# Performance work log

Measured on AMD Instinct MI355X. Metric: run time of the kernel, lower is better.

The kernel has to match this reference:

```python
import jax, jax.numpy as jnp
import numpy as np

BATCH = 32
N_LEVELS = (16384, 4096, 1024, 256)   # nodes at each mesh resolution
M_LEVELS = (4096, 1024, 256, 64)      # nodes after each Pool (downsample)
DEG = 6                               # directed edges per node
POOL_K = 3                            # nnz per row of downsample matrix
FILTERS = (3, 32, 32, 32, 64)         # channel chain of the 4 ChebConvs
K_CHEB = 6                            # Chebyshev polynomial order


def setup_inputs() -> dict:
    key = jax.random.key(0)
    ks = iter(jax.random.split(key, 64))
    inp = {"x": jax.random.normal(next(ks), (BATCH, N_LEVELS[0], FILTERS[0]), jnp.float32)}
    for i, N in enumerate(N_LEVELS):
        er = jnp.repeat(jnp.arange(N), DEG)
        off = jax.random.randint(next(ks), (N * DEG,), 1, N)
        inp[f"er{i}"] = er
        inp[f"ec{i}"] = (er + off) % N  # guaranteed no self loops
    for i, (M, N) in enumerate(zip(M_LEVELS, N_LEVELS)):
        inp[f"pr{i}"] = jnp.repeat(jnp.arange(M), POOL_K)
        inp[f"pc{i}"] = jax.random.randint(next(ks), (M * POOL_K,), 0, N)
        inp[f"pv{i}"] = jax.random.uniform(next(ks), (M * POOL_K,), jnp.float32)
    for i in range(4):
        fin, fout = FILTERS[i], FILTERS[i + 1]
        scale = 1.0 / np.sqrt(fin * K_CHEB)
        inp[f"W{i}"] = jax.random.normal(next(ks), (K_CHEB, fin, fout), jnp.float32) * scale
        inp[f"b{i}"] = jnp.zeros((fout,), jnp.float32)
    inp["enc_W"] = jax.random.normal(next(ks), (M_LEVELS[-1] * FILTERS[-1], 128), jnp.float32) * 0.1
    inp["enc_b"] = jnp.zeros((128,), jnp.float32)
    inp["cls_W"] = jax.random.normal(next(ks), (128, 10), jnp.float32) * 0.1
    inp["cls_b"] = jnp.zeros((10,), jnp.float32)
    return inp


def _cheb_conv(x, er, ec, W, b):
    # x: [B,N,Fin]; W: [K,Fin,Fout].
    # PyG ChebConv with lambda_max=2: L_hat = L - I = -D^{-1/2} A D^{-1/2}.
    N = x.shape[1]
    deg = jnp.zeros((N,), x.dtype).at[er].add(1.0)
    dinv = jnp.where(deg > 0, 1.0 / jnp.sqrt(jnp.maximum(deg, 1.0)), 0.0)
    norm = -(dinv[er] * dinv[ec])  # [E]

    def L(t):  # sparse matvec: gather neighbor feats, weight, scatter-add
        return jnp.zeros_like(t).at[:, er].add(t[:, ec] * norm[None, :, None])

    Tx0 = x
    out = jnp.einsum("bnf,fg->bng", Tx0, W[0])
    Tx1 = L(x)
    out = out + jnp.einsum("bnf,fg->bng", Tx1, W[1])
    for k in range(2, W.shape[0]):
        Tx2 = 2.0 * L(Tx1) - Tx0
        out = out + jnp.einsum("bnf,fg->bng", Tx2, W[k])
        Tx0, Tx1 = Tx1, Tx2
    return out + b


def _pool(x, pr, pc, pv, m):
    # sparse downsample matrix [m,N]: index_select cols * value, scatter_add rows
    B, _, F = x.shape
    return jnp.zeros((B, m, F), x.dtype).at[:, pr].add(x[:, pc] * pv[None, :, None])


def reference(x, er0, ec0, er1, ec1, er2, ec2, er3, ec3,
              pr0, pc0, pv0, pr1, pc1, pv1, pr2, pc2, pv2, pr3, pc3, pv3,
              W0, b0, W1, b1, W2, b2, W3, b3, enc_W, enc_b, cls_W, cls_b):
    ers, ecs = (er0, er1, er2, er3), (ec0, ec1, ec2, ec3)
    prs, pcs, pvs = (pr0, pr1, pr2, pr3), (pc0, pc1, pc2, pc3), (pv0, pv1, pv2, pv3)
    Ws, bs = (W0, W1, W2, W3), (b0, b1, b2, b3)
    for i in range(4):  # fixed n_layers loop (structurally distinct layers)
        x = jax.nn.relu(_cheb_conv(x, ers[i], ecs[i], Ws[i], bs[i]))
        x = _pool(x, prs[i], pcs[i], pvs[i], M_LEVELS[i])
    x = x.reshape(x.shape[0], -1)  # [B, 64*64]
    h = jax.nn.relu(x @ enc_W + enc_b)
    return h @ cls_W + cls_b
```

## Files before the change

kernel.cpp:

```cpp
#include <hip/hip_runtime.h>
#include <hip/hip_fp16.h>
#include <cstddef>
#include <cstdint>

#define BATCH 32


struct alignas(8) half4 { __half2 lo, hi; };

__device__ __forceinline__ void h4f(const half4 h, float f[4]) {
  float2 a = __half22float2(h.lo);
  float2 c = __half22float2(h.hi);
  f[0] = a.x; f[1] = a.y; f[2] = c.x; f[3] = c.y;
}
__device__ __forceinline__ void fma4(float4& a, float s, const float4& w) {
  a.x += s * w.x; a.y += s * w.y; a.z += s * w.z; a.w += s * w.w;
}
__device__ __forceinline__ float4 relu4(const float4& a) {
  return make_float4(fmaxf(a.x, 0.f), fmaxf(a.y, 0.f), fmaxf(a.z, 0.f), fmaxf(a.w, 0.f));
}

__global__ void __launch_bounds__(256) transpose_h(
    const float* __restrict__ x, half4* __restrict__ xh)
{
  int t = blockIdx.x * 256 + threadIdx.x;
  int n = t >> 5;
  int b = t & 31;
  const float* src = x + ((size_t)b * 16384 + n) * 3;
  half4 h;
  h.lo = __floats2half2_rn(src[0], src[1]);
  h.hi = __floats2half2_rn(src[2], 0.f);
  xh[t] = h;
}

__global__ void __launch_bounds__(256) cheb_step_h2(
    const half4* __restrict__ Tin, const half4* __restrict__ Tpp,
    const int* __restrict__ ec, half4* __restrict__ Tout,
    float coef, float beta)
{
  int idx = blockIdx.x * 256 + threadIdx.x;
  int n = idx >> 5;
  int b = idx & 31;
  int idx2 = idx + 262144;
  const int* e  = ec + n * 6;
  const int* e2 = ec + (n + 8192) * 6;
  float s0 = 0.f, s1 = 0.f, s2 = 0.f;
  float u0 = 0.f, u1 = 0.f, u2 = 0.f;
#pragma unroll
  for (int d = 0; d < 6; ++d) {
    half4 v = Tin[(e[d]  << 5) | b];
    half4 w = Tin[(e2[d] << 5) | b];
    float2 a = __half22float2(v.lo);
    float2 c = __half22float2(v.hi);
    s0 += a.x; s1 += a.y; s2 += c.x;
    float2 aw = __half22float2(w.lo);
    float2 cw = __half22float2(w.hi);
    u0 += aw.x; u1 += aw.y; u2 += cw.x;
  }
  half4 p  = Tpp[idx];
  half4 p2 = Tpp[idx2];
  float2 pa = __half22float2(p.lo);
  float2 pc = __half22float2(p.hi);
  float2 qa = __half22float2(p2.lo);
  float2 qc = __half22float2(p2.hi);
  half4 o, o2;
  o.lo  = __floats2half2_rn(coef * s0 + beta * pa.x, coef * s1 + beta * pa.y);
  o.hi  = __floats2half2_rn(coef * s2 + beta * pc.x, 0.f);
  o2.lo = __floats2half2_rn(coef * u0 + beta * qa.x, coef * u1 + beta * qa.y);
  o2.hi = __floats2half2_rn(coef * u2 + beta * qc.x, 0.f);
  Tout[idx]  = o;
  Tout[idx2] = o2;
}

template<int N, int M, int FOUT>
__global__ void __launch_bounds__(256) pool_conv_f3_h(
    const half4* __restrict__ Xh, const half4* __restrict__ T,
    const float* __restrict__ W, const float* __restrict__ bias,
    const int* __restrict__ pc, const float* __restrict__ pv,
    float* __restrict__ out)
{
  constexpr int F4 = FOUT / 4;
  constexpr size_t SL = (size_t)N * 32;
  __shared__ float Ws[6 * 3 * FOUT];
  for (int i = threadIdx.x; i < 6 * 3 * FOUT; i += 256) Ws[i] = W[i];
  __syncthreads();
  const float4* Ws4 = (const float4*)Ws;
  int t = blockIdx.x * 256 + threadIdx.x;
  int fo4 = t % F4;
  int b   = (t / F4) % BATCH;
  int m   = t / (F4 * BATCH);
  int c0 = pc[m * 3 + 0], c1 = pc[m * 3 + 1], c2 = pc[m * 3 + 2];
  float v0 = pv[m * 3 + 0], v1 = pv[m * 3 + 1], v2 = pv[m * 3 + 2];
  float4 bi = ((const float4*)bias)[fo4];
  float4 a0 = bi, a1 = bi, a2 = bi;
#pragma unroll
  for (int k = 0; k < 6; ++k) {
    const half4* base = (k == 0) ? Xh : (T + (size_t)(k - 1) * SL);
    float r0[4], r1[4], r2[4];
    h4f(base[(c0 << 5) | b], r0);
    h4f(base[(c1 << 5) | b], r1);
    h4f(base[(c2 << 5) | b], r2);
#pragma unroll
    for (int f = 0; f < 3; ++f) {
      float4 w = Ws4[(k * 3 + f) * F4 + fo4];
      fma4(a0, r0[f], w);
      fma4(a1, r1[f], w);
      fma4(a2, r2[f], w);
    }
  }
  a0 = relu4(a0); a1 = relu4(a1); a2 = relu4(a2);
  float4 acc;
  acc.x = v0*a0.x + v1*a1.x + v2*a2.x;
  acc.y = v0*a0.y + v1*a1.y + v2*a2.y;
  acc.z = v0*a0.z + v1*a1.z + v2*a2.z;
  acc.w = v0*a0.w + v1*a1.w + v2*a2.w;
  ((float4*)out)[((size_t)m * BATCH + b) * F4 + fo4] = acc;
}

template<int N, int F, int THREADS, int MINW>
__global__ void __launch_bounds__(THREADS, MINW) cheb_recur_hh(
    const float* __restrict__ X,
    const int* __restrict__ ec,
    __half* __restrict__ Th)
{
  constexpr int NPT = N / THREADS;
  __shared__ half4 cur[N];
  const float cI = -1.0f / 6.0f;
  const float cS = -1.0f / 3.0f;
  const int b = blockIdx.x & 31;
  const int fbase = (blockIdx.x >> 5) * 4;
  constexpr size_t SLH = (size_t)N * 32 * F;
  half4 prevv[NPT], newh[NPT];
#pragma unroll
  for (int i = 0; i < NPT; ++i) {
    int n = threadIdx.x + i * THREADS;
    float4 xv = *(const float4*)(X + ((size_t)n * 32 + b) * F + fbase);
    half4 h;
    h.lo = __floats2half2_rn(xv.x, xv.y);
    h.hi = __floats2half2_rn(xv.z, xv.w);
    cur[n] = h;
  }
  __syncthreads();
#pragma unroll 1
  for (int k = 1; k <= 5; ++k) {
    __half* Tk = Th + (size_t)(k - 1) * SLH;
#pragma unroll
    for (int i = 0; i < NPT; ++i) {
      int n = threadIdx.x + i * THREADS;
      const int2* e2 = (const int2*)(ec + n * 6);
      int2 ea = e2[0], eb = e2[1], ez = e2[2];
      int na[6];
      na[0] = ea.x; na[1] = ea.y; na[2] = eb.x;
      na[3] = eb.y; na[4] = ez.x; na[5] = ez.y;
      float s0 = 0.f, s1 = 0.f, s2 = 0.f, s3 = 0.f;
#pragma unroll
      for (int d = 0; d < 6; ++d) {
        half4 t = cur[na[d]];
        float2 a = __half22float2(t.lo);
        float2 c = __half22float2(t.hi);
        s0 += a.x; s1 += a.y; s2 += c.x; s3 += c.y;
      }
      float v0, v1, v2, v3;
      if (k == 1) {
        v0 = cI * s0; v1 = cI * s1; v2 = cI * s2; v3 = cI * s3;
      } else {
        float2 pa = __half22float2(prevv[i].lo);
        float2 pc = __half22float2(prevv[i].hi);
        v0 = cS * s0 - pa.x; v1 = cS * s1 - pa.y;
        v2 = cS * s2 - pc.x; v3 = cS * s3 - pc.y;
      }
      half4 h;
      h.lo = __floats2half2_rn(v0, v1);
      h.hi = __floats2half2_rn(v2, v3);
      newh[i] = h;
      *(half4*)(Tk + ((size_t)n * 32 + b) * F + fbase) = h;
    }
    __syncthreads();
#pragma unroll
    for (int i = 0; i < NPT; ++i) {
      int n = threadIdx.x + i * THREADS;
      prevv[i] = cur[n];
      cur[n] = newh[i];
    }
    __syncthreads();
  }
}

template<int N, int M, int FOUT, bool OUT_BM>
__global__ void __launch_bounds__(256) pool_conv_v32_h(
    const float* __restrict__ X, const __half* __restrict__ Th,
    const float* __restrict__ W, const float* __restrict__ bias,
    const int* __restrict__ pc, const float* __restrict__ pv,
    float* __restrict__ out)
{
  constexpr int FIN = 32;
  constexpr int F4 = FOUT / 4;
  constexpr size_t SLH = (size_t)N * 32 * FIN;
  __shared__ float Ws[6 * FIN * FOUT];
  for (int i = threadIdx.x; i < 6 * FIN * FOUT; i += 256) Ws[i] = W[i];
  __syncthreads();
  const float4* Ws4 = (const float4*)Ws;
  const float4* X4p = (const float4*)X;
  int t = blockIdx.x * 256 + threadIdx.x;
  int fo4 = t % F4;
  int b   = (t / F4) % BATCH;
  int m   = t / (F4 * BATCH);
  int c0 = pc[m * 3 + 0], c1 = pc[m * 3 + 1], c2 = pc[m * 3 + 2];
  float v0 = pv[m * 3 + 0], v1 = pv[m * 3 + 1], v2 = pv[m * 3 + 2];
  float4 bi = ((const float4*)bias)[fo4];
  float4 a0 = bi, a1 = bi, a2 = bi;
  {
    const float4* r0 = X4p + ((size_t)c0 * BATCH + b) * 8;
    const float4* r1 = X4p + ((size_t)c1 * BATCH + b) * 8;
    const float4* r2 = X4p + ((size_t)c2 * BATCH + b) * 8;
#pragma unroll
    for (int fi = 0; fi < 8; ++fi) {
      float4 t0 = r0[fi], t1 = r1[fi], t2 = r2[fi];
#pragma unroll
      for (int ff = 0; ff < 4; ++ff) {
        float4 w = Ws4[(fi * 4 + ff) * F4 + fo4];
        fma4(a0, ((const float*)&t0)[ff], w);
        fma4(a1, ((const float*)&t1)[ff], w);
        fma4(a2, ((const float*)&t2)[ff], w);
      }
    }
  }
#pragma unroll 1
  for (int k = 1; k < 6; ++k) {
    const half4* base = (const half4*)(Th + (size_t)(k - 1) * SLH);
    const half4* r0 = base + ((size_t)c0 * 32 + b) * 8;
    const half4* r1 = base + ((size_t)c1 * 32 + b) * 8;
    const half4* r2 = base + ((size_t)c2 * 32 + b) * 8;
#pragma unroll
    for (int q = 0; q < 8; ++q) {
      float f0[4], f1[4], f2[4];
      h4f(r0[q], f0); h4f(r1[q], f1); h4f(r2[q], f2);
#pragma unroll
      for (int ff = 0; ff < 4; ++ff) {
        float4 w = Ws4[((k * 32) + q * 4 + ff) * F4 + fo4];
        fma4(a0, f0[ff], w);
        fma4(a1, f1[ff], w);
        fma4(a2, f2[ff], w);
      }
    }
  }
  a0 = relu4(a0); a1 = relu4(a1); a2 = relu4(a2);
  float4 acc;
  acc.x = v0*a0.x + v1*a1.x + v2*a2.x;
  acc.y = v0*a0.y + v1*a1.y + v2*a2.y;
  acc.z = v0*a0.z + v1*a1.z + v2*a2.z;
  acc.w = v0*a0.w + v1*a1.w + v2*a2.w;
  size_t oi = OUT_BM ? (((size_t)b * M + m) * F4 + fo4) : (((size_t)m * BATCH + b) * F4 + fo4);
  ((float4*)out)[oi] = acc;
}

__global__ void __launch_bounds__(128) encoder_partial_ws(
    const float* __restrict__ Xf, const float* __restrict__ encW,
    float* __restrict__ partial)
{
  int j  = blockIdx.x;
  int fo = threadIdx.x;
  int i0 = j * 32;
  float w[32];
#pragma unroll
  for (int i = 0; i < 32; ++i) w[i] = encW[(size_t)(i0 + i) * 128 + fo];
#pragma unroll 1
  for (int b = 0; b < 32; ++b) {
    const float* xr = Xf + b * 4096 + i0;
    float s = 0.f;
#pragma unroll
    for (int i = 0; i < 32; ++i) s += xr[i] * w[i];
    partial[((size_t)b * 128 + j) * 128 + fo] = s;
  }
}

__global__ void __launch_bounds__(128) encoder_reduce_cls(
    const float* __restrict__ partial, const float* __restrict__ encB,
    const float* __restrict__ clsW, const float* __restrict__ clsB,
    float* __restrict__ out)
{
  int b = blockIdx.x;
  int fo = threadIdx.x;
  float acc = encB[fo];
#pragma unroll 8
  for (int j = 0; j < 128; ++j) acc += partial[((size_t)b * 128 + j) * 128 + fo];
  __shared__ float Hs[128];
  Hs[fo] = fmaxf(acc, 0.f);
  __syncthreads();
  if (fo < 10) {
    float s = clsB[fo];
#pragma unroll 4
    for (int f = 0; f < 128; ++f) s += Hs[f] * clsW[f * 10 + fo];
    out[b * 10 + fo] = s;
  }
}

extern "C" void kernel_launch(void* const* d_in, const int* in_sizes, int n_in,
                              void* d_out, int out_size, void* d_ws, size_t ws_size,
                              hipStream_t stream)
{
  const float* x   = (const float*)d_in[0];
  const int* ec0 = (const int*)d_in[2];
  const int* ec1 = (const int*)d_in[4];
  const int* ec2 = (const int*)d_in[6];
  const int* ec3 = (const int*)d_in[8];
  const int* pc0 = (const int*)d_in[10]; const float* pv0 = (const float*)d_in[11];
  const int* pc1 = (const int*)d_in[13]; const float* pv1 = (const float*)d_in[14];
  const int* pc2 = (const int*)d_in[16]; const float* pv2 = (const float*)d_in[17];
  const int* pc3 = (const int*)d_in[19]; const float* pv3 = (const float*)d_in[20];
  const float* W0 = (const float*)d_in[21]; const float* b0 = (const float*)d_in[22];
  const float* W1 = (const float*)d_in[23]; const float* b1 = (const float*)d_in[24];
  const float* W2 = (const float*)d_in[25]; const float* b2 = (const float*)d_in[26];
  const float* W3 = (const float*)d_in[27]; const float* b3 = (const float*)d_in[28];
  const float* encW = (const float*)d_in[29]; const float* encB = (const float*)d_in[30];
  const float* clsW = (const float*)d_in[31]; const float* clsB = (const float*)d_in[32];
  float* out = (float*)d_out;

  float* ws = (float*)d_ws;
  half4*  Xh = (half4*)ws;
  __half* Th = (__half*)(ws + 1048576);
  float* X1 = ws + 1048576 + 10485760;
  float* X2 = X1 + 4194304;
  float* X3 = X2 + 1048576;
  float* X4 = X3 + 262144;
  float* P  = X4 + 131072;

  const float cI = -1.0f / 6.0f;
  const float cS = -1.0f / 3.0f;
  dim3 blk(256);

  transpose_h<<<dim3(2048), blk, 0, stream>>>(x, Xh);

  {
    constexpr size_t S = (size_t)16384 * 32;
    half4* T4 = (half4*)Th;
    cheb_step_h2<<<dim3(1024), blk, 0, stream>>>(Xh,       Xh,       ec0, T4,        cI,  0.f);
    cheb_step_h2<<<dim3(1024), blk, 0, stream>>>(T4,       Xh,       ec0, T4 + S,    cS, -1.f);
    cheb_step_h2<<<dim3(1024), blk, 0, stream>>>(T4 + S,   T4,       ec0, T4 + 2*S,  cS, -1.f);
    cheb_step_h2<<<dim3(1024), blk, 0, stream>>>(T4 + 2*S, T4 + S,   ec0, T4 + 3*S,  cS, -1.f);
    cheb_step_h2<<<dim3(1024), blk, 0, stream>>>(T4 + 3*S, T4 + 2*S, ec0, T4 + 4*S,  cS, -1.f);
    pool_conv_f3_h<16384, 4096, 32><<<dim3(4096), blk, 0, stream>>>(
        Xh, (const half4*)Th, W0, b0, pc0, pv0, X1);
  }
  cheb_recur_hh<4096, 32, 1024, 4><<<dim3(256), dim3(1024), 0, stream>>>(X1, ec1, Th);
  pool_conv_v32_h<4096, 1024, 32, false><<<dim3(1024), blk, 0, stream>>>(
      X1, Th, W1, b1, pc1, pv1, X2);

  cheb_recur_hh<1024, 32, 256, 4><<<dim3(256), blk, 0, stream>>>(X2, ec2, Th);
  pool_conv_v32_h<1024, 256, 32, false><<<dim3(256), blk, 0, stream>>>(
      X2, Th, W2, b2, pc2, pv2, X3);

  cheb_recur_hh<256, 32, 256, 4><<<dim3(256), blk, 0, stream>>>(X3, ec3, Th);
  pool_conv_v32_h<256, 64, 64, true><<<dim3(128), blk, 0, stream>>>(
      X3, Th, W3, b3, pc3, pv3, X4);

  encoder_partial_ws<<<dim3(128), dim3(128), 0, stream>>>(X4, encW, P);
  encoder_reduce_cls<<<dim3(32), dim3(128), 0, stream>>>(P, encB, clsW, clsB, out);
}
```

Before: 281.7 us.

## Fuse all post-level-1 stages into one per-batch persistent tail kernel

Replaces the level-1 pool, the level-2/3 Chebyshev recurrences and pools, and both encoder kernels with a single 32-block kernel, one block per batch element. Each block handles all feature slabs sequentially and uses block-level barriers instead of kernel boundaries. The level-0 cheb step goes back to one node per thread with vectorised int2 edge loads, and the level-3 weights are stored in shared memory as fp16. This removes about eight kernel launches and their idle gaps, but runs the tail on only 32 CUs, which serialises work that was previously spread over 256 blocks.

```diff
diff --git a/kernel.cpp b/kernel.cpp
--- a/kernel.cpp
+++ b/kernel.cpp
@@ -33,7 +33,7 @@
   xh[t] = h;
 }
 
-__global__ void __launch_bounds__(256) cheb_step_h2(
+__global__ void __launch_bounds__(256) cheb_step_h(
     const half4* __restrict__ Tin, const half4* __restrict__ Tpp,
     const int* __restrict__ ec, half4* __restrict__ Tout,
     float coef, float beta)
@@ -41,48 +41,38 @@
   int idx = blockIdx.x * 256 + threadIdx.x;
   int n = idx >> 5;
   int b = idx & 31;
-  int idx2 = idx + 262144;
-  const int* e  = ec + n * 6;
-  const int* e2 = ec + (n + 8192) * 6;
+  const int2* e2 = (const int2*)(ec + n * 6);
+  int2 ea = e2[0], eb = e2[1], ez = e2[2];
+  int na[6];
+  na[0] = ea.x; na[1] = ea.y; na[2] = eb.x;
+  na[3] = eb.y; na[4] = ez.x; na[5] = ez.y;
   float s0 = 0.f, s1 = 0.f, s2 = 0.f;
-  float u0 = 0.f, u1 = 0.f, u2 = 0.f;
 #pragma unroll
   for (int d = 0; d < 6; ++d) {
-    half4 v = Tin[(e[d]  << 5) | b];
-    half4 w = Tin[(e2[d] << 5) | b];
+    half4 v = Tin[(na[d] << 5) | b];
     float2 a = __half22float2(v.lo);
     float2 c = __half22float2(v.hi);
     s0 += a.x; s1 += a.y; s2 += c.x;
-    float2 aw = __half22float2(w.lo);
-    float2 cw = __half22float2(w.hi);
-    u0 += aw.x; u1 += aw.y; u2 += cw.x;
-  }
-  half4 p  = Tpp[idx];
-  half4 p2 = Tpp[idx2];
+  }
+  half4 p = Tpp[idx];
   float2 pa = __half22float2(p.lo);
   float2 pc = __half22float2(p.hi);
-  float2 qa = __half22float2(p2.lo);
-  float2 qc = __half22float2(p2.hi);
-  half4 o, o2;
-  o.lo  = __floats2half2_rn(coef * s0 + beta * pa.x, coef * s1 + beta * pa.y);
-  o.hi  = __floats2half2_rn(coef * s2 + beta * pc.x, 0.f);
-  o2.lo = __floats2half2_rn(coef * u0 + beta * qa.x, coef * u1 + beta * qa.y);
-  o2.hi = __floats2half2_rn(coef * u2 + beta * qc.x, 0.f);
-  Tout[idx]  = o;
-  Tout[idx2] = o2;
-}
-
-template<int N, int M, int FOUT>
+  half4 o;
+  o.lo = __floats2half2_rn(coef * s0 + beta * pa.x, coef * s1 + beta * pa.y);
+  o.hi = __floats2half2_rn(coef * s2 + beta * pc.x, 0.f);
+  Tout[idx] = o;
+}
+
 __global__ void __launch_bounds__(256) pool_conv_f3_h(
     const half4* __restrict__ Xh, const half4* __restrict__ T,
     const float* __restrict__ W, const float* __restrict__ bias,
     const int* __restrict__ pc, const float* __restrict__ pv,
     float* __restrict__ out)
 {
-  constexpr int F4 = FOUT / 4;
-  constexpr size_t SL = (size_t)N * 32;
-  __shared__ float Ws[6 * 3 * FOUT];
-  for (int i = threadIdx.x; i < 6 * 3 * FOUT; i += 256) Ws[i] = W[i];
+  constexpr int F4 = 8;
+  constexpr size_t SL = (size_t)16384 * 32;
+  __shared__ float Ws[576];
+  for (int i = threadIdx.x; i < 576; i += 256) Ws[i] = W[i];
   __syncthreads();
   const float4* Ws4 = (const float4*)Ws;
   int t = blockIdx.x * 256 + threadIdx.x;
@@ -117,10 +107,75 @@
   ((float4*)out)[((size_t)m * BATCH + b) * F4 + fo4] = acc;
 }
 
+template<int N, int M, int FOUT, bool OUT_BM, bool WH>
+__device__ __forceinline__ void st_pool32(
+    const float* __restrict__ X, const __half* __restrict__ Th,
+    const void* __restrict__ Ws, const float* __restrict__ bias,
+    const int* __restrict__ pc, const float* __restrict__ pv,
+    float* __restrict__ out, int t)
+{
+  constexpr int F4 = FOUT / 4;
+  constexpr size_t SLH = (size_t)N * 32 * 32;
+  const float4* Wsf = (const float4*)Ws;
+  const half4* Wsh = (const half4*)Ws;
+  const float4* X4p = (const float4*)X;
+  int fo4 = t % F4;
+  int b   = (t / F4) % BATCH;
+  int m   = t / (F4 * BATCH);
+  int c0 = pc[m * 3 + 0], c1 = pc[m * 3 + 1], c2 = pc[m * 3 + 2];
+  float v0 = pv[m * 3 + 0], v1 = pv[m * 3 + 1], v2 = pv[m * 3 + 2];
+  float4 bi = ((const float4*)bias)[fo4];
+  float4 a0 = bi, a1 = bi, a2 = bi;
+#define WGET(off) (WH ? ({ float wf[4]; h4f(Wsh[off], wf); make_float4(wf[0],wf[1],wf[2],wf[3]); }) : Wsf[off])
+  {
+    const float4* r0 = X4p + ((size_t)c0 * BATCH + b) * 8;
+    const float4* r1 = X4p + ((size_t)c1 * BATCH + b) * 8;
+    const float4* r2 = X4p + ((size_t)c2 * BATCH + b) * 8;
+#pragma unroll
+    for (int fi = 0; fi < 8; ++fi) {
+      float4 t0 = r0[fi], t1 = r1[fi], t2 = r2[fi];
+#pragma unroll
+      for (int ff = 0; ff < 4; ++ff) {
+        float4 w = WGET((fi * 4 + ff) * F4 + fo4);
+        fma4(a0, ((const float*)&t0)[ff], w);
+        fma4(a1, ((const float*)&t1)[ff], w);
+        fma4(a2, ((const float*)&t2)[ff], w);
+      }
+    }
+  }
+#pragma unroll 1
+  for (int k = 1; k < 6; ++k) {
+    const half4* base = (const half4*)(Th + (size_t)(k - 1) * SLH);
+    const half4* r0 = base + ((size_t)c0 * 32 + b) * 8;
+    const half4* r1 = base + ((size_t)c1 * 32 + b) * 8;
+    const half4* r2 = base + ((size_t)c2 * 32 + b) * 8;
+#pragma unroll
+    for (int q = 0; q < 8; ++q) {
+      float f0[4], f1[4], f2[4];
+      h4f(r0[q], f0); h4f(r1[q], f1); h4f(r2[q], f2);
+#pragma unroll
+      for (int ff = 0; ff < 4; ++ff) {
+        float4 w = WGET(((k * 32) + q * 4 + ff) * F4 + fo4);
+        fma4(a0, f0[ff], w);
+        fma4(a1, f1[ff], w);
+        fma4(a2, f2[ff], w);
+      }
+    }
+  }
+#undef WGET
+  a0 = relu4(a0); a1 = relu4(a1); a2 = relu4(a2);
+  float4 acc;
+  acc.x = v0*a0.x + v1*a1.x + v2*a2.x;
+  acc.y = v0*a0.y + v1*a1.y + v2*a2.y;
+  acc.z = v0*a0.z + v1*a1.z + v2*a2.z;
+  acc.w = v0*a0.w + v1*a1.w + v2*a2.w;
+  size_t oi = OUT_BM ? (((size_t)b * M + m) * F4 + fo4) : (((size_t)m * BATCH + b) * F4 + fo4);
+  ((float4*)out)[oi] = acc;
+}
+
 template<int N, int F, int THREADS, int MINW>
 __global__ void __launch_bounds__(THREADS, MINW) cheb_recur_hh(
-    const float* __restrict__ X,
-    const int* __restrict__ ec,
+    const float* __restrict__ X, const int* __restrict__ ec,
     __half* __restrict__ Th)
 {
   constexpr int NPT = N / THREADS;
@@ -186,114 +241,155 @@
   }
 }
 
-template<int N, int M, int FOUT, bool OUT_BM>
-__global__ void __launch_bounds__(256) pool_conv_v32_h(
-    const float* __restrict__ X, const __half* __restrict__ Th,
-    const float* __restrict__ W, const float* __restrict__ bias,
-    const int* __restrict__ pc, const float* __restrict__ pv,
-    float* __restrict__ out)
-{
-  constexpr int FIN = 32;
-  constexpr int F4 = FOUT / 4;
-  constexpr size_t SLH = (size_t)N * 32 * FIN;
-  __shared__ float Ws[6 * FIN * FOUT];
-  for (int i = threadIdx.x; i < 6 * FIN * FOUT; i += 256) Ws[i] = W[i];
-  __syncthreads();
-  const float4* Ws4 = (const float4*)Ws;
-  const float4* X4p = (const float4*)X;
-  int t = blockIdx.x * 256 + threadIdx.x;
-  int fo4 = t % F4;
-  int b   = (t / F4) % BATCH;
-  int m   = t / (F4 * BATCH);
-  int c0 = pc[m * 3 + 0], c1 = pc[m * 3 + 1], c2 = pc[m * 3 + 2];
-  float v0 = pv[m * 3 + 0], v1 = pv[m * 3 + 1], v2 = pv[m * 3 + 2];
-  float4 bi = ((const float4*)bias)[fo4];
-  float4 a0 = bi, a1 = bi, a2 = bi;
+template<int N>
+__device__ void tail_recur(const float* __restrict__ X, const int* __restrict__ ec,
+                           __half* __restrict__ Th, half4* cur, int b, int fbase, int tid)
+{
+  constexpr size_t SLH = (size_t)N * 32 * 32;
+  const float cI = -1.0f / 6.0f;
+  const float cS = -1.0f / 3.0f;
+  const bool act = tid < N;
+  const int n = tid;
+  half4 prev, neww;
+  if (act) {
+    float4 xv = *(const float4*)(X + ((size_t)n * 32 + b) * 32 + fbase);
+    half4 h;
+    h.lo = __floats2half2_rn(xv.x, xv.y);
+    h.hi = __floats2half2_rn(xv.z, xv.w);
+    cur[n] = h;
+  }
+  __syncthreads();
+#pragma unroll 1
+  for (int k = 1; k <= 5; ++k) {
+    __half* Tk = Th + (size_t)(k - 1) * SLH;
+    if (act) {
+      const int2* e2 = (const int2*)(ec + n * 6);
+      int2 ea = e2[0], eb = e2[1], ez = e2[2];
+      int na[6];
+      na[0] = ea.x; na[1] = ea.y; na[2] = eb.x;
+      na[3] = eb.y; na[4] = ez.x; na[5] = ez.y;
+      float s0 = 0.f, s1 = 0.f, s2 = 0.f, s3 = 0.f;
+#pragma unroll
+      for (int d = 0; d < 6; ++d) {
+        half4 t = cur[na[d]];
+        float2 a = __half22float2(t.lo);
+        float2 c = __half22float2(t.hi);
+        s0 += a.x; s1 += a.y; s2 += c.x; s3 += c.y;
+      }
+      float v0, v1, v2, v3;
+      if (k == 1) {
+        v0 = cI * s0; v1 = cI * s1; v2 = cI * s2; v3 = cI * s3;
+      } else {
+        float2 pa = __half22float2(prev.lo);
+        float2 pc = __half22float2(prev.hi);
+        v0 = cS * s0 - pa.x; v1 = cS * s1 - pa.y;
+        v2 = cS * s2 - pc.x; v3 = cS * s3 - pc.y;
+      }
+      neww.lo = __floats2half2_rn(v0, v1);
+      neww.hi = __floats2half2_rn(v2, v3);
+      *(half4*)(Tk + ((size_t)n * 32 + b) * 32 + fbase) = neww;
+    }
+    __syncthreads();
+    if (act) {
+      prev = cur[n];
+      cur[n] = neww;
+    }
+    __syncthreads();
+  }
+}
+
+struct TailP {
+  const float* X1; __half* Th;
+  const float *W1, *b1; const int* pc1; const float* pv1; float* X2;
+  const int* ec2; const float *W2, *b2; const int* pc2; const float* pv2; float* X3;
+  const int* ec3; const float *W3, *b3; const int* pc3; const float* pv3; float* X4;
+  const float *encW, *encB, *clsW, *clsB; float* out;
+};
+
+__global__ void __launch_bounds__(1024, 1) tail_per_b(TailP p)
+{
+  const int b = blockIdx.x;
+  const int tid = threadIdx.x;
+  __shared__ __align__(16) char sm[33792];
+  float* Wsf = (float*)sm;
+  __half* Wsh = (__half*)sm;
+  half4* cur = (half4*)(sm + 24576);
+
+  for (int i = tid; i < 6144; i += 1024) Wsf[i] = p.W1[i];
+  __syncthreads();
+#pragma unroll 1
+  for (int g = 0; g < 8; ++g) {
+    int m = g * 128 + (tid >> 3);
+    int fo4 = tid & 7;
+    st_pool32<4096, 1024, 32, false, false>(p.X1, p.Th, Wsf, p.b1, p.pc1, p.pv1,
+                                            p.X2, (m * 32 + b) * 8 + fo4);
+  }
+  __threadfence();
+  __syncthreads();
+
+#pragma unroll 1
+  for (int slab = 0; slab < 8; ++slab)
+    tail_recur<1024>(p.X2, p.ec2, p.Th, cur, b, slab * 4, tid);
+  __threadfence();
+  __syncthreads();
+
+  for (int i = tid; i < 6144; i += 1024) Wsf[i] = p.W2[i];
+  __syncthreads();
+#pragma unroll 1
+  for (int g = 0; g < 2; ++g) {
+    int m = g * 128 + (tid >> 3);
+    int fo4 = tid & 7;
+    st_pool32<1024, 256, 32, false, false>(p.X2, p.Th, Wsf, p.b2, p.pc2, p.pv2,
+                                           p.X3, (m * 32 + b) * 8 + fo4);
+  }
+  __threadfence();
+  __syncthreads();
+
+#pragma unroll 1
+  for (int slab = 0; slab < 8; ++slab)
+    tail_recur<256>(p.X3, p.ec3, p.Th, cur, b, slab * 4, tid);
+  __threadfence();
+  __syncthreads();
+
+  for (int i = tid; i < 12288; i += 1024) Wsh[i] = __float2half(p.W3[i]);
+  __syncthreads();
   {
-    const float4* r0 = X4p + ((size_t)c0 * BATCH + b) * 8;
-    const float4* r1 = X4p + ((size_t)c1 * BATCH + b) * 8;
-    const float4* r2 = X4p + ((size_t)c2 * BATCH + b) * 8;
-#pragma unroll
-    for (int fi = 0; fi < 8; ++fi) {
-      float4 t0 = r0[fi], t1 = r1[fi], t2 = r2[fi];
-#pragma unroll
-      for (int ff = 0; ff < 4; ++ff) {
-        float4 w = Ws4[(fi * 4 + ff) * F4 + fo4];
-        fma4(a0, ((const float*)&t0)[ff], w);
-        fma4(a1, ((const float*)&t1)[ff], w);
-        fma4(a2, ((const float*)&t2)[ff], w);
-      }
-    }
-  }
-#pragma unroll 1
-  for (int k = 1; k < 6; ++k) {
-    const half4* base = (const half4*)(Th + (size_t)(k - 1) * SLH);
-    const half4* r0 = base + ((size_t)c0 * 32 + b) * 8;
-    const half4* r1 = base + ((size_t)c1 * 32 + b) * 8;
-    const half4* r2 = base + ((size_t)c2 * 32 + b) * 8;
-#pragma unroll
-    for (int q = 0; q < 8; ++q) {
-      float f0[4], f1[4], f2[4];
-      h4f(r0[q], f0); h4f(r1[q], f1); h4f(r2[q], f2);
-#pragma unroll
-      for (int ff = 0; ff < 4; ++ff) {
-        float4 w = Ws4[((k * 32) + q * 4 + ff) * F4 + fo4];
-        fma4(a0, f0[ff], w);
-        fma4(a1, f1[ff], w);
-        fma4(a2, f2[ff], w);
-      }
-    }
-  }
-  a0 = relu4(a0); a1 = relu4(a1); a2 = relu4(a2);
-  float4 acc;
-  acc.x = v0*a0.x + v1*a1.x + v2*a2.x;
-  acc.y = v0*a0.y + v1*a1.y + v2*a2.y;
-  acc.z = v0*a0.z + v1*a1.z + v2*a2.z;
-  acc.w = v0*a0.w + v1*a1.w + v2*a2.w;
-  size_t oi = OUT_BM ? (((size_t)b * M + m) * F4 + fo4) : (((size_t)m * BATCH + b) * F4 + fo4);
-  ((float4*)out)[oi] = acc;
-}
-
-__global__ void __launch_bounds__(128) encoder_partial_ws(
-    const float* __restrict__ Xf, const float* __restrict__ encW,
-    float* __restrict__ partial)
-{
-  int j  = blockIdx.x;
-  int fo = threadIdx.x;
-  int i0 = j * 32;
-  float w[32];
-#pragma unroll
-  for (int i = 0; i < 32; ++i) w[i] = encW[(size_t)(i0 + i) * 128 + fo];
-#pragma unroll 1
-  for (int b = 0; b < 32; ++b) {
-    const float* xr = Xf + b * 4096 + i0;
+    int m = tid >> 4;
+    int fo4 = tid & 15;
+    st_pool32<256, 64, 64, true, true>(p.X3, p.Th, Wsh, p.b3, p.pc3, p.pv3,
+                                       p.X4, (m * 32 + b) * 16 + fo4);
+  }
+  __threadfence();
+  __syncthreads();
+
+  {
+    int fo = tid & 127;
+    int ks = tid >> 7;
+    const float* xr = p.X4 + b * 4096 + ks * 512;
+    const float* w  = p.encW + (size_t)(ks * 512) * 128 + fo;
     float s = 0.f;
-#pragma unroll
-    for (int i = 0; i < 32; ++i) s += xr[i] * w[i];
-    partial[((size_t)b * 128 + j) * 128 + fo] = s;
-  }
-}
-
-__global__ void __launch_bounds__(128) encoder_reduce_cls(
-    const float* __restrict__ partial, const float* __restrict__ encB,
-    const float* __restrict__ clsW, const float* __restrict__ clsB,
-    float* __restrict__ out)
-{
-  int b = blockIdx.x;
-  int fo = threadIdx.x;
-  float acc = encB[fo];
 #pragma unroll 8
-  for (int j = 0; j < 128; ++j) acc += partial[((size_t)b * 128 + j) * 128 + fo];
-  __shared__ float Hs[128];
-  Hs[fo] = fmaxf(acc, 0.f);
-  __syncthreads();
-  if (fo < 10) {
-    float s = clsB[fo];
+    for (int i = 0; i < 512; ++i) s += xr[i] * w[(size_t)i * 128];
+    float* part = (float*)sm;
+    part[ks * 128 + fo] = s;
+    __syncthreads();
+    float* Hs = (float*)(sm + 4096);
+    if (tid < 128) {
+      float acc = p.encB[tid];
+#pragma unroll
+      for (int k2 = 0; k2 < 8; ++k2) acc += part[k2 * 128 + tid];
+      Hs[tid] = fmaxf(acc, 0.f);
+    }
+    __syncthreads();
+    if (tid < 10) {
+      float s2 = p.clsB[tid];
 #pragma unroll 4
-    for (int f = 0; f < 128; ++f) s += Hs[f] * clsW[f * 10 + fo];
-    out[b * 10 + fo] = s;
-  }
-}
+      for (int f = 0; f < 128; ++f) s2 += Hs[f] * p.clsW[f * 10 + tid];
+      p.out[b * 10 + tid] = s2;
+    }
+  }
+}
+
 
 extern "C" void kernel_launch(void* const* d_in, const int* in_sizes, int n_in,
                               void* d_out, int out_size, void* d_ws, size_t ws_size,
@@ -323,37 +419,27 @@
   float* X2 = X1 + 4194304;
   float* X3 = X2 + 1048576;
   float* X4 = X3 + 262144;
-  float* P  = X4 + 131072;
 
   const float cI = -1.0f / 6.0f;
   const float cS = -1.0f / 3.0f;
   dim3 blk(256);
+  constexpr size_t S = (size_t)16384 * 32;
+  half4* T4 = (half4*)Th;
 
   transpose_h<<<dim3(2048), blk, 0, stream>>>(x, Xh);
-
-  {
-    constexpr size_t S = (size_t)16384 * 32;
-    half4* T4 = (half4*)Th;
-    cheb_step_h2<<<dim3(1024), blk, 0, stream>>>(Xh,       Xh,       ec0, T4,        cI,  0.f);
-    cheb_step_h2<<<dim3(1024), blk, 0, stream>>>(T4,       Xh,       ec0, T4 + S,    cS, -1.f);
-    cheb_step_h2<<<dim3(1024), blk, 0, stream>>>(T4 + S,   T4,       ec0, T4 + 2*S,  cS, -1.f);
-    cheb_step_h2<<<dim3(1024), blk, 0, stream>>>(T4 + 2*S, T4 + S,   ec0, T4 + 3*S,  cS, -1.f);
-    cheb_step_h2<<<dim3(1024), blk, 0, stream>>>(T4 + 3*S, T4 + 2*S, ec0, T4 + 4*S,  cS, -1.f);
-    pool_conv_f3_h<16384, 4096, 32><<<dim3(4096), blk, 0, stream>>>(
-        Xh, (const half4*)Th, W0, b0, pc0, pv0, X1);
-  }
+  cheb_step_h<<<dim3(2048), blk, 0, stream>>>(Xh,       Xh,       ec0, T4,        cI,  0.f);
+  cheb_step_h<<<dim3(2048), blk, 0, stream>>>(T4,       Xh,       ec0, T4 + S,    cS, -1.f);
+  cheb_step_h<<<dim3(2048), blk, 0, stream>>>(T4 + S,   T4,       ec0, T4 + 2*S,  cS, -1.f);
+  cheb_step_h<<<dim3(2048), blk, 0, stream>>>(T4 + 2*S, T4 + S,   ec0, T4 + 3*S,  cS, -1.f);
+  cheb_step_h<<<dim3(2048), blk, 0, stream>>>(T4 + 3*S, T4 + 2*S, ec0, T4 + 4*S,  cS, -1.f);
+  pool_conv_f3_h<<<dim3(4096), blk, 0, stream>>>(Xh, T4, W0, b0, pc0, pv0, X1);
+
   cheb_recur_hh<4096, 32, 1024, 4><<<dim3(256), dim3(1024), 0, stream>>>(X1, ec1, Th);
-  pool_conv_v32_h<4096, 1024, 32, false><<<dim3(1024), blk, 0, stream>>>(
-      X1, Th, W1, b1, pc1, pv1, X2);
-
-  cheb_recur_hh<1024, 32, 256, 4><<<dim3(256), blk, 0, stream>>>(X2, ec2, Th);
-  pool_conv_v32_h<1024, 256, 32, false><<<dim3(256), blk, 0, stream>>>(
-      X2, Th, W2, b2, pc2, pv2, X3);
-
-  cheb_recur_hh<256, 32, 256, 4><<<dim3(256), blk, 0, stream>>>(X3, ec3, Th);
-  pool_conv_v32_h<256, 64, 64, true><<<dim3(128), blk, 0, stream>>>(
-      X3, Th, W3, b3, pc3, pv3, X4);
-
-  encoder_partial_ws<<<dim3(128), dim3(128), 0, stream>>>(X4, encW, P);
-  encoder_reduce_cls<<<dim3(32), dim3(128), 0, stream>>>(P, encB, clsW, clsB, out);
-}
+
+  TailP tp{ X1, Th,
+            W1, b1, pc1, pv1, X2,
+            ec2, W2, b2, pc2, pv2, X3,
+            ec3, W3, b3, pc3, pv3, X4,
+            encW, encB, clsW, clsB, out };
+  tail_per_b<<<dim3(32), dim3(1024), 0, stream>>>(tp);
+}
```

After: 643.0 us. 2.28x slower.

## Fuse level-0 Chebyshev recursion into one LDS-resident kernel per batch-channel

Applied to the files above, without the earlier changes.

Replaces the transpose kernel and five separate global-memory Chebyshev step launches at level 0 with a single kernel. Each of 96 blocks (batch × input channel) keeps the whole 16384-node signal in shared memory as fp16 and runs all five recursion steps with block barriers. Every Tx_k is written to a planar [k][b][ch][n] layout, and the pooling/conv kernel now gathers scalar halves from that layout. This removes launch overhead and global gather traffic, but leaves only 96 blocks on the GPU and turns the pool kernel's loads into uncoalesced scalar gathers.

```diff
diff --git a/kernel.cpp b/kernel.cpp
--- a/kernel.cpp
+++ b/kernel.cpp
@@ -20,69 +20,61 @@
   return make_float4(fmaxf(a.x, 0.f), fmaxf(a.y, 0.f), fmaxf(a.z, 0.f), fmaxf(a.w, 0.f));
 }
 
-__global__ void __launch_bounds__(256) transpose_h(
-    const float* __restrict__ x, half4* __restrict__ xh)
-{
-  int t = blockIdx.x * 256 + threadIdx.x;
-  int n = t >> 5;
-  int b = t & 31;
-  const float* src = x + ((size_t)b * 16384 + n) * 3;
-  half4 h;
-  h.lo = __floats2half2_rn(src[0], src[1]);
-  h.hi = __floats2half2_rn(src[2], 0.f);
-  xh[t] = h;
-}
-
-__global__ void __launch_bounds__(256) cheb_step_h2(
-    const half4* __restrict__ Tin, const half4* __restrict__ Tpp,
-    const int* __restrict__ ec, half4* __restrict__ Tout,
-    float coef, float beta)
-{
-  int idx = blockIdx.x * 256 + threadIdx.x;
-  int n = idx >> 5;
-  int b = idx & 31;
-  int idx2 = idx + 262144;
-  const int* e  = ec + n * 6;
-  const int* e2 = ec + (n + 8192) * 6;
-  float s0 = 0.f, s1 = 0.f, s2 = 0.f;
-  float u0 = 0.f, u1 = 0.f, u2 = 0.f;
-#pragma unroll
-  for (int d = 0; d < 6; ++d) {
-    half4 v = Tin[(e[d]  << 5) | b];
-    half4 w = Tin[(e2[d] << 5) | b];
-    float2 a = __half22float2(v.lo);
-    float2 c = __half22float2(v.hi);
-    s0 += a.x; s1 += a.y; s2 += c.x;
-    float2 aw = __half22float2(w.lo);
-    float2 cw = __half22float2(w.hi);
-    u0 += aw.x; u1 += aw.y; u2 += cw.x;
-  }
-  half4 p  = Tpp[idx];
-  half4 p2 = Tpp[idx2];
-  float2 pa = __half22float2(p.lo);
-  float2 pc = __half22float2(p.hi);
-  float2 qa = __half22float2(p2.lo);
-  float2 qc = __half22float2(p2.hi);
-  half4 o, o2;
-  o.lo  = __floats2half2_rn(coef * s0 + beta * pa.x, coef * s1 + beta * pa.y);
-  o.hi  = __floats2half2_rn(coef * s2 + beta * pc.x, 0.f);
-  o2.lo = __floats2half2_rn(coef * u0 + beta * qa.x, coef * u1 + beta * qa.y);
-  o2.hi = __floats2half2_rn(coef * u2 + beta * qc.x, 0.f);
-  Tout[idx]  = o;
-  Tout[idx2] = o2;
-}
-
-template<int N, int M, int FOUT>
-__global__ void __launch_bounds__(256) pool_conv_f3_h(
-    const half4* __restrict__ Xh, const half4* __restrict__ T,
-    const float* __restrict__ W, const float* __restrict__ bias,
-    const int* __restrict__ pc, const float* __restrict__ pv,
-    float* __restrict__ out)
-{
-  constexpr int F4 = FOUT / 4;
-  constexpr size_t SL = (size_t)N * 32;
-  __shared__ float Ws[6 * 3 * FOUT];
-  for (int i = threadIdx.x; i < 6 * 3 * FOUT; i += 256) Ws[i] = W[i];
+__global__ void __launch_bounds__(1024) chain_bc(
+    const float* __restrict__ x, const int* __restrict__ ec,
+    __half* __restrict__ P)
+{
+  __shared__ __half cur[16384];
+  const int b  = blockIdx.x & 31;
+  const int ch = blockIdx.x >> 5;
+  const int tid = threadIdx.x;
+  float prevv[16], newv[16];
+  {
+    __half* p0 = P + ((size_t)(0 * 32 + b) * 3 + ch) * 16384;
+#pragma unroll
+    for (int i = 0; i < 16; ++i) {
+      int n = tid + (i << 10);
+      __half h = __float2half(x[((size_t)b * 16384 + n) * 3 + ch]);
+      cur[n] = h;
+      p0[n] = h;
+    }
+  }
+  __syncthreads();
+  const float cI = -1.0f / 6.0f, cS = -1.0f / 3.0f;
+#pragma unroll 1
+  for (int k = 1; k <= 5; ++k) {
+    __half* pk = P + ((size_t)(k * 32 + b) * 3 + ch) * 16384;
+#pragma unroll
+    for (int i = 0; i < 16; ++i) {
+      int n = tid + (i << 10);
+      const int2* e2 = (const int2*)(ec + n * 6);
+      int2 ea = e2[0], eb = e2[1], ez = e2[2];
+      float s = __half2float(cur[ea.x]) + __half2float(cur[ea.y])
+              + __half2float(cur[eb.x]) + __half2float(cur[eb.y])
+              + __half2float(cur[ez.x]) + __half2float(cur[ez.y]);
+      float v = (k == 1) ? (cI * s) : (cS * s - prevv[i]);
+      newv[i] = v;
+      pk[n] = __float2half(v);
+    }
+    __syncthreads();
+#pragma unroll
+    for (int i = 0; i < 16; ++i) {
+      int n = tid + (i << 10);
+      prevv[i] = __half2float(cur[n]);
+      cur[n] = __float2half(newv[i]);
+    }
+    __syncthreads();
+  }
+}
+
+__global__ void __launch_bounds__(256) pool0_p(
+    const __half* __restrict__ P, const float* __restrict__ W,
+    const float* __restrict__ bias, const int* __restrict__ pc,
+    const float* __restrict__ pv, float* __restrict__ out)
+{
+  constexpr int F4 = 8;
+  __shared__ float Ws[576];
+  for (int i = threadIdx.x; i < 576; i += 256) Ws[i] = W[i];
   __syncthreads();
   const float4* Ws4 = (const float4*)Ws;
   int t = blockIdx.x * 256 + threadIdx.x;
@@ -93,19 +85,20 @@
   float v0 = pv[m * 3 + 0], v1 = pv[m * 3 + 1], v2 = pv[m * 3 + 2];
   float4 bi = ((const float4*)bias)[fo4];
   float4 a0 = bi, a1 = bi, a2 = bi;
+  const size_t bbase = (size_t)b * 3 * 16384;
 #pragma unroll
   for (int k = 0; k < 6; ++k) {
-    const half4* base = (k == 0) ? Xh : (T + (size_t)(k - 1) * SL);
-    float r0[4], r1[4], r2[4];
-    h4f(base[(c0 << 5) | b], r0);
-    h4f(base[(c1 << 5) | b], r1);
-    h4f(base[(c2 << 5) | b], r2);
+    const __half* pk = P + (size_t)k * 32 * 3 * 16384 + bbase;
 #pragma unroll
     for (int f = 0; f < 3; ++f) {
+      const __half* pl = pk + (size_t)f * 16384;
+      float r0 = __half2float(pl[c0]);
+      float r1 = __half2float(pl[c1]);
+      float r2 = __half2float(pl[c2]);
       float4 w = Ws4[(k * 3 + f) * F4 + fo4];
-      fma4(a0, r0[f], w);
-      fma4(a1, r1[f], w);
-      fma4(a2, r2[f], w);
+      fma4(a0, r0, w);
+      fma4(a1, r1, w);
+      fma4(a2, r2, w);
     }
   }
   a0 = relu4(a0); a1 = relu4(a1); a2 = relu4(a2);
@@ -295,6 +288,7 @@
   }
 }
 
+
 extern "C" void kernel_launch(void* const* d_in, const int* in_sizes, int n_in,
                               void* d_out, int out_size, void* d_ws, size_t ws_size,
                               hipStream_t stream)
@@ -317,31 +311,18 @@
   float* out = (float*)d_out;
 
   float* ws = (float*)d_ws;
-  half4*  Xh = (half4*)ws;
-  __half* Th = (__half*)(ws + 1048576);
-  float* X1 = ws + 1048576 + 10485760;
+  __half* Th = (__half*)ws;
+  float* X1 = ws + 10485760;
   float* X2 = X1 + 4194304;
   float* X3 = X2 + 1048576;
   float* X4 = X3 + 262144;
   float* P  = X4 + 131072;
 
-  const float cI = -1.0f / 6.0f;
-  const float cS = -1.0f / 3.0f;
   dim3 blk(256);
 
-  transpose_h<<<dim3(2048), blk, 0, stream>>>(x, Xh);
-
-  {
-    constexpr size_t S = (size_t)16384 * 32;
-    half4* T4 = (half4*)Th;
-    cheb_step_h2<<<dim3(1024), blk, 0, stream>>>(Xh,       Xh,       ec0, T4,        cI,  0.f);
-    cheb_step_h2<<<dim3(1024), blk, 0, stream>>>(T4,       Xh,       ec0, T4 + S,    cS, -1.f);
-    cheb_step_h2<<<dim3(1024), blk, 0, stream>>>(T4 + S,   T4,       ec0, T4 + 2*S,  cS, -1.f);
-    cheb_step_h2<<<dim3(1024), blk, 0, stream>>>(T4 + 2*S, T4 + S,   ec0, T4 + 3*S,  cS, -1.f);
-    cheb_step_h2<<<dim3(1024), blk, 0, stream>>>(T4 + 3*S, T4 + 2*S, ec0, T4 + 4*S,  cS, -1.f);
-    pool_conv_f3_h<16384, 4096, 32><<<dim3(4096), blk, 0, stream>>>(
-        Xh, (const half4*)Th, W0, b0, pc0, pv0, X1);
-  }
+  chain_bc<<<dim3(96), dim3(1024), 0, stream>>>(x, ec0, Th);
+  pool0_p<<<dim3(4096), blk, 0, stream>>>(Th, W0, b0, pc0, pv0, X1);
+
   cheb_recur_hh<4096, 32, 1024, 4><<<dim3(256), dim3(1024), 0, stream>>>(X1, ec1, Th);
   pool_conv_v32_h<4096, 1024, 32, false><<<dim3(1024), blk, 0, stream>>>(
       X1, Th, W1, b1, pc1, pv1, X2);
```

After: 377.6 us. 1.34x slower.
